# Kernel tuning notes

Hardware: AMD Instinct MI355X
Metric: run time of the kernel (lower is better)

Reference implementation:

```python
import jax, jax.numpy as jnp
import numpy as np

NUM_COMPONENTS = 4
HEADS = 16

def setup_inputs() -> dict:
    key = jax.random.key(0)
    ks = jax.random.split(key, 7)
    BC, S, D = 8, 4096, 1024   # batch*components, latent tokens, hidden dim
    E = 160                     # encoder (text) sequence length
    w_scale = 0.02              # keep logits in a sane range
    return {
        "hidden_states": jax.random.normal(ks[0], (BC, S, D), jnp.float32),
        "encoder_hidden_states": jax.random.normal(ks[1], (BC, E, D), jnp.float32),
        "Wq": jax.random.normal(ks[2], (D, D), jnp.float32) * w_scale,
        "Wk": jax.random.normal(ks[3], (D, D), jnp.float32) * w_scale,
        "Wv": jax.random.normal(ks[4], (D, D), jnp.float32) * w_scale,
        "Wo": jax.random.normal(ks[5], (D, D), jnp.float32) * w_scale,
        "bo": jnp.zeros((D,), jnp.float32),
    }

def reference(hidden_states, encoder_hidden_states, Wq, Wk, Wv, Wo, bo):
    BC, S, D = hidden_states.shape
    E = encoder_hidden_states.shape[1]
    C = NUM_COMPONENTS
    B = BC // C
    H = HEADS
    dh = D // H
    scale = dh ** -0.5

    # projections (diffusers to_q/to_k/to_v, no bias)
    q = hidden_states @ Wq            # [BC, S, D]
    k = encoder_hidden_states @ Wk    # [BC, E, D]
    v = encoder_hidden_states @ Wv    # [BC, E, D]

    q = q.reshape(BC, S, H, dh).transpose(0, 2, 1, 3)  # [BC, H, S, dh]
    k = k.reshape(BC, E, H, dh).transpose(0, 2, 1, 3)  # [BC, H, E, dh]
    v = v.reshape(BC, E, H, dh).transpose(0, 2, 1, 3)  # [BC, H, E, dh]

    scores = jnp.einsum("bhsd,bhtd->bhst", q, k) * scale  # [BC, H, S, E]
    scores_c = scores.reshape(C, B, H, S, E)

    # pooled (mean over encoder tokens) softmax across components
    pooled = scores_c.mean(axis=-1, keepdims=True)         # [C, B, H, S, 1]
    weights_pooled = jax.nn.softmax(pooled, axis=0)        # softmax over components
    # per-row softmax over encoder tokens, scaled by component weight
    weights = jax.nn.softmax(scores_c, axis=-1) * weights_pooled
    weights = weights.reshape(BC, H, S, E)

    out = jnp.einsum("bhst,bhtd->bhsd", weights, v)        # [BC, H, S, dh]
    out = out.transpose(0, 2, 1, 3).reshape(BC, S, D)

    out = out @ Wo + bo        # to_out[0]; to_out[1] is dropout (identity, eval)
    out = out + hidden_states  # residual_connection=True, rescale factor 1
    return out
```

## Files before the change

### kernel.cpp

```cpp
#include <hip/hip_runtime.h>
#include <stdint.h>

typedef __attribute__((ext_vector_type(8))) short short8;
typedef __attribute__((ext_vector_type(4))) float f32x4;
typedef __attribute__((ext_vector_type(4))) unsigned short us4;

#define DI __device__ __forceinline__

static constexpr int Dm = 1024;
static constexpr int Sm = 4096;
static constexpr int Em = 160;
static constexpr int Hm = 16;

static constexpr size_t OFF_HSB  = 0;
static constexpr size_t OFF_WT   = 67108864;
static constexpr size_t OFF_QB   = 75497472;
static constexpr size_t OFF_KB   = 142606336;
static constexpr size_t OFF_VT   = 147849216;
static constexpr size_t OFF_EHSB = 150994944;

DI unsigned short f2b(float f) {
  union { float f; unsigned u; } x; x.f = f;
  unsigned r = x.u + 0x7fffu + ((x.u >> 16) & 1u);
  return (unsigned short)(r >> 16);
}

DI float b2f(unsigned short h) {
  union { unsigned u; float f; } x; x.u = ((unsigned)h) << 16; return x.f;
}

DI void gl_lds16(const void* g, void* l) {
  __builtin_amdgcn_global_load_lds(
      (const __attribute__((address_space(1))) unsigned int*)g,
      (__attribute__((address_space(3))) unsigned int*)l, 16, 0, 0);
}

__global__ void k_prep(const float* __restrict__ ehs, unsigned short* __restrict__ eb,
                       const float* __restrict__ hs, unsigned short* __restrict__ hsb,
                       const float* __restrict__ W0, const float* __restrict__ W1,
                       const float* __restrict__ W2, const float* __restrict__ W3,
                       unsigned short* __restrict__ Wt) {
  __shared__ float t[32][33];
  const int bid = blockIdx.x, tid = threadIdx.x;
  if (bid < 4096) {
    const int bz = bid >> 10, rest = bid & 1023, by = rest >> 5, bx = rest & 31;
    const float* W = (bz == 0) ? W0 : (bz == 1) ? W1 : (bz == 2) ? W2 : W3;
    unsigned short* o = Wt + (size_t)bz * 1048576;
    const int tx = tid & 31, ty = tid >> 5;
    const int n = bx * 32 + tx, k0 = by * 32;
    #pragma unroll
    for (int j = ty; j < 32; j += 8) t[j][tx] = W[(size_t)(k0 + j) * 1024 + n];
    __syncthreads();
    #pragma unroll
    for (int j = ty; j < 32; j += 8)
      o[(size_t)(bx * 32 + j) * 1024 + k0 + tx] = f2b(t[tx][j]);
  } else if (bid < 5376) {
    const int i = (bid - 4096) * 256 + tid;
    float4 v = ((const float4*)ehs)[i];
    us4 o = { f2b(v.x), f2b(v.y), f2b(v.z), f2b(v.w) };
    *(us4*)(eb + (size_t)i * 4) = o;
  } else {
    for (int i = (bid - 5376) * 256 + tid; i < 8388608; i += 2048 * 256) {
      float4 v = ((const float4*)hs)[i];
      us4 o = { f2b(v.x), f2b(v.y), f2b(v.z), f2b(v.w) };
      *(us4*)(hsb + (size_t)i * 4) = o;
    }
  }
}

__global__ __launch_bounds__(256, 3) void k_gemm_qkv(const unsigned short* __restrict__ hsb,
                                                     const unsigned short* __restrict__ eb,
                                                     const unsigned short* __restrict__ Wt,
                                                     unsigned short* __restrict__ qb,
                                                     unsigned short* __restrict__ kb,
                                                     unsigned short* __restrict__ vt) {
  __shared__ __align__(16) char smem[32768];
  char* As = smem;
  char* Bs = smem + 16384;
  const int bid = blockIdx.x, tid = threadIdx.x;
  const int lane = tid & 63;
  const int l15 = lane & 15;
  const int g = lane >> 4;
  const int wv = tid >> 6;
  const int wr = wv >> 1, wc = wv & 1;

  const bool isKV = (bid < 160);
  int m0, n0;
  const unsigned short *Ap, *Bt;
  if (isKV) {
    const int z = bid / 80, rr = bid - z * 80;
    m0 = (rr % 10) * 128; n0 = (rr / 10) * 128;
    Ap = eb; Bt = Wt + (size_t)(1 + z) * 1048576;
  } else {
    const int q = bid - 160;
    m0 = ((q >> 6) * 8 + (q & 7)) * 128;
    n0 = ((q >> 3) & 7) * 128;
    Ap = hsb; Bt = Wt;
  }

  f32x4 acc[4][4];
  #pragma unroll
  for (int i = 0; i < 4; ++i)
    #pragma unroll
    for (int j = 0; j < 4; ++j) acc[i][j] = (f32x4){0.f, 0.f, 0.f, 0.f};

  for (int t = 0; t < 16; ++t) {
    __syncthreads();
    #pragma unroll
    for (int is = 0; is < 4; ++is) {
      int ch = is * 256 + tid;
      int row = ch >> 3, j = ch & 7;
      int sj = (j ^ (row & 7)) * 8;
      gl_lds16(Ap + (size_t)(m0 + row) * 1024 + t * 64 + sj, As + ch * 16);
      gl_lds16(Bt + (size_t)(n0 + row) * 1024 + t * 64 + sj, Bs + ch * 16);
    }
    __syncthreads();
    short8 af[2][4], bf[2][4];
    #pragma unroll
    for (int kk = 0; kk < 2; ++kk)
      #pragma unroll
      for (int mt = 0; mt < 4; ++mt) {
        af[kk][mt] = *(const short8*)(As + (wr * 64 + mt * 16 + l15) * 128 + ((kk * 64 + g * 16) ^ ((l15 & 7) << 4)));
        bf[kk][mt] = *(const short8*)(Bs + (wc * 64 + mt * 16 + l15) * 128 + ((kk * 64 + g * 16) ^ ((l15 & 7) << 4)));
      }
    #pragma unroll
    for (int kk = 0; kk < 2; ++kk)
      #pragma unroll
      for (int mt = 0; mt < 4; ++mt)
        #pragma unroll
        for (int nt = 0; nt < 4; ++nt)
          acc[mt][nt] = __builtin_amdgcn_mfma_f32_16x16x32_bf16(af[kk][mt], bf[kk][nt], acc[mt][nt], 0, 0, 0);
  }

  if (isKV) {
    const int z = bid / 80;
    #pragma unroll
    for (int mt = 0; mt < 4; ++mt)
      #pragma unroll
      for (int nt = 0; nt < 4; ++nt)
        #pragma unroll
        for (int r = 0; r < 4; ++r) {
          int row = m0 + wr * 64 + mt * 16 + 4 * g + r;
          int col = n0 + wc * 64 + nt * 16 + l15;
          unsigned short hv = f2b(acc[mt][nt][r]);
          if (z == 0) {
            kb[(size_t)row * 1024 + col] = hv;
          } else {
            int bc = row / 160, e = row - bc * 160;
            vt[((size_t)(bc * 16 + (col >> 6)) * 64 + (col & 63)) * 192 + e] = hv;
          }
        }
  } else {
    __syncthreads();
    unsigned short* Cl = (unsigned short*)smem;
    #pragma unroll
    for (int mt = 0; mt < 4; ++mt)
      #pragma unroll
      for (int nt = 0; nt < 4; ++nt)
        #pragma unroll
        for (int r = 0; r < 4; ++r)
          Cl[(wr * 64 + mt * 16 + 4 * g + r) * 128 + wc * 64 + nt * 16 + l15] = f2b(acc[mt][nt][r]);
    __syncthreads();
    #pragma unroll
    for (int j = 0; j < 8; ++j) {
      int ch = j * 256 + tid;
      int row = ch >> 4, sl = ch & 15;
      __builtin_nontemporal_store(*(const short8*)(Cl + row * 128 + sl * 8),
          (short8*)(qb + (size_t)(m0 + row) * 1024 + n0 + sl * 8));
    }
  }
}

__global__ __launch_bounds__(256, 3) void k_gemm_o(const unsigned short* __restrict__ A,
                                                   const unsigned short* __restrict__ Bt,
                                                   float* __restrict__ Cout,
                                                   const float* __restrict__ bias,
                                                   const unsigned short* __restrict__ residb) {
  __shared__ __align__(16) char smem[32768];
  char* As = smem;
  char* Bs = smem + 16384;
  const int tid = threadIdx.x;
  const int lane = tid & 63;
  const int l15 = lane & 15;
  const int g = lane >> 4;
  const int wv = tid >> 6;
  const int wr = wv >> 1, wc = wv & 1;
  const int bid = blockIdx.x;
  const int m0 = ((bid >> 6) * 8 + (bid & 7)) * 128;
  const int n0 = ((bid >> 3) & 7) * 128;

  f32x4 acc[4][4];
  #pragma unroll
  for (int i = 0; i < 4; ++i)
    #pragma unroll
    for (int j = 0; j < 4; ++j) acc[i][j] = (f32x4){0.f, 0.f, 0.f, 0.f};

  for (int t = 0; t < 16; ++t) {
    __syncthreads();
    #pragma unroll
    for (int is = 0; is < 4; ++is) {
      int ch = is * 256 + tid;
      int row = ch >> 3, j = ch & 7;
      int sj = (j ^ (row & 7)) * 8;
      gl_lds16(A  + (size_t)(m0 + row) * 1024 + t * 64 + sj, As + ch * 16);
      gl_lds16(Bt + (size_t)(n0 + row) * 1024 + t * 64 + sj, Bs + ch * 16);
    }
    __syncthreads();
    short8 af[2][4], bf[2][4];
    #pragma unroll
    for (int kk = 0; kk < 2; ++kk)
      #pragma unroll
      for (int mt = 0; mt < 4; ++mt) {
        af[kk][mt] = *(const short8*)(As + (wr * 64 + mt * 16 + l15) * 128 + ((kk * 64 + g * 16) ^ ((l15 & 7) << 4)));
        bf[kk][mt] = *(const short8*)(Bs + (wc * 64 + mt * 16 + l15) * 128 + ((kk * 64 + g * 16) ^ ((l15 & 7) << 4)));
      }
    #pragma unroll
    for (int kk = 0; kk < 2; ++kk)
      #pragma unroll
      for (int mt = 0; mt < 4; ++mt)
        #pragma unroll
        for (int nt = 0; nt < 4; ++nt)
          acc[mt][nt] = __builtin_amdgcn_mfma_f32_16x16x32_bf16(af[kk][mt], bf[kk][nt], acc[mt][nt], 0, 0, 0);
  }

  #pragma unroll
  for (int mt = 0; mt < 4; ++mt)
    #pragma unroll
    for (int nt = 0; nt < 4; ++nt)
      #pragma unroll
      for (int r = 0; r < 4; ++r) {
        size_t row = (size_t)(m0 + wr * 64 + mt * 16 + 4 * g + r);
        int col = n0 + wc * 64 + nt * 16 + l15;
        size_t idx = row * 1024 + col;
        unsigned short rh = __builtin_nontemporal_load(residb + idx);
        Cout[idx] = acc[mt][nt][r] + bias[col] + b2f(rh);
      }
}

__global__ __launch_bounds__(256, 2) void k_attn(unsigned short* __restrict__ Qb,
                                                 const unsigned short* __restrict__ Kb,
                                                 const unsigned short* __restrict__ Vt) {
  __shared__ __align__(16) char smem[22528];
  float* pooled = (float*)(smem + 21504);
  const int tid = threadIdx.x, lane = tid & 63, wv = tid >> 6;
  const int g = lane >> 4, l15 = lane & 15;
  const int s0 = blockIdx.x * 64;
  const int h = blockIdx.y;
  const int b = blockIdx.z;
  const int bc = wv * 2 + b;
  const float scale = 0.125f;

  unsigned short* Qp = Qb + ((size_t)bc * Sm + s0) * Dm + h * 64;
  const unsigned short* Kp = Kb + (size_t)bc * Em * Dm + h * 64;
  const unsigned short* Vp = Vt + ((size_t)bc * Hm + h) * (64 * 192);
  char* Pw = smem + wv * 5376;

  #pragma unroll 1
  for (int st = 0; st < 4; ++st) {
    short8 qf[2];
    #pragma unroll
    for (int kk = 0; kk < 2; ++kk)
      qf[kk] = *(const short8*)(Qp + (size_t)(st * 16 + l15) * Dm + kk * 32 + g * 8);
    f32x4 sc[10];
    #pragma unroll
    for (int et = 0; et < 10; ++et) {
      sc[et] = (f32x4){0.f, 0.f, 0.f, 0.f};
      #pragma unroll
      for (int kk = 0; kk < 2; ++kk) {
        short8 kf = *(const short8*)(Kp + (size_t)(et * 16 + l15) * Dm + kk * 32 + g * 8);
        sc[et] = __builtin_amdgcn_mfma_f32_16x16x32_bf16(qf[kk], kf, sc[et], 0, 0, 0);
      }
    }
    float rs4[4];
    #pragma unroll
    for (int r = 0; r < 4; ++r) {
      float v = 0.f;
      #pragma unroll
      for (int et = 0; et < 10; ++et) v += sc[et][r];
      v += __shfl_xor(v, 1); v += __shfl_xor(v, 2); v += __shfl_xor(v, 4); v += __shfl_xor(v, 8);
      if (l15 == 0) pooled[(st * 16 + 4 * g + r) * 4 + wv] = v * (scale / 160.f);
      float mx = sc[0][r];
      #pragma unroll
      for (int et = 1; et < 10; ++et) mx = fmaxf(mx, sc[et][r]);
      mx = fmaxf(mx, __shfl_xor(mx, 1)); mx = fmaxf(mx, __shfl_xor(mx, 2));
      mx = fmaxf(mx, __shfl_xor(mx, 4)); mx = fmaxf(mx, __shfl_xor(mx, 8));
      float rs = 0.f;
      #pragma unroll
      for (int et = 0; et < 10; ++et) {
        float p = __expf((sc[et][r] - mx) * scale);
        rs += p;
        *(unsigned short*)(Pw + (4 * g + r) * 336 + (et * 16 + l15) * 2) = f2b(p);
      }
      rs += __shfl_xor(rs, 1); rs += __shfl_xor(rs, 2); rs += __shfl_xor(rs, 4); rs += __shfl_xor(rs, 8);
      rs4[r] = rs;
    }
    f32x4 oa[4];
    #pragma unroll
    for (int dt = 0; dt < 4; ++dt) oa[dt] = (f32x4){0.f, 0.f, 0.f, 0.f};
    #pragma unroll
    for (int k5 = 0; k5 < 5; ++k5) {
      short8 pf = *(const short8*)(Pw + l15 * 336 + k5 * 64 + g * 16);
      #pragma unroll
      for (int dt = 0; dt < 4; ++dt) {
        short8 vf = *(const short8*)(Vp + (size_t)(dt * 16 + l15) * 192 + k5 * 32 + g * 8);
        oa[dt] = __builtin_amdgcn_mfma_f32_16x16x32_bf16(pf, vf, oa[dt], 0, 0, 0);
      }
    }
    __syncthreads();
    #pragma unroll
    for (int r = 0; r < 4; ++r) {
      float4 pl = *(const float4*)&pooled[(st * 16 + 4 * g + r) * 4];
      float m3 = fmaxf(fmaxf(pl.x, pl.y), fmaxf(pl.z, pl.w));
      float ssum = __expf(pl.x - m3) + __expf(pl.y - m3) + __expf(pl.z - m3) + __expf(pl.w - m3);
      float mine = (wv == 0) ? pl.x : (wv == 1) ? pl.y : (wv == 2) ? pl.z : pl.w;
      float srw = __expf(mine - m3) / (ssum * rs4[r]);
      #pragma unroll
      for (int dt = 0; dt < 4; ++dt)
        Qp[(size_t)(st * 16 + 4 * g + r) * Dm + dt * 16 + l15] = f2b(oa[dt][r] * srw);
    }
  }
}

extern "C" void kernel_launch(void* const* d_in, const int* in_sizes, int n_in,
                              void* d_out, int out_size, void* d_ws, size_t ws_size,
                              hipStream_t stream) {
  const float* hs  = (const float*)d_in[0];
  const float* ehs = (const float*)d_in[1];
  const float* Wq  = (const float*)d_in[2];
  const float* Wk  = (const float*)d_in[3];
  const float* Wv  = (const float*)d_in[4];
  const float* Wo  = (const float*)d_in[5];
  const float* bo  = (const float*)d_in[6];
  char* ws = (char*)d_ws;
  unsigned short* hsb = (unsigned short*)(ws + OFF_HSB);
  unsigned short* wt  = (unsigned short*)(ws + OFF_WT);
  unsigned short* qb  = (unsigned short*)(ws + OFF_QB);
  unsigned short* kb  = (unsigned short*)(ws + OFF_KB);
  unsigned short* vt  = (unsigned short*)(ws + OFF_VT);
  unsigned short* eb  = (unsigned short*)(ws + OFF_EHSB);

  hipLaunchKernelGGL(k_prep, dim3(7424), dim3(256), 0, stream, ehs, eb, hs, hsb, Wq, Wk, Wv, Wo, wt);
  hipLaunchKernelGGL(k_gemm_qkv, dim3(2208), dim3(256), 0, stream, hsb, eb, wt, qb, kb, vt);
  hipLaunchKernelGGL(k_attn, dim3(64, 16, 2), dim3(256), 0, stream, qb, kb, vt);
  hipLaunchKernelGGL(k_gemm_o, dim3(2048), dim3(256), 0, stream, qb, wt + 3 * 1048576, (float*)d_out, bo, hsb);
}
```

Before: 334.2 us.

## Compute pooled scores via mean-key MFMA and drop softmax max subtraction

```diff
diff --git a/kernel.cpp b/kernel.cpp
--- a/kernel.cpp
+++ b/kernel.cpp
@@ -16,6 +16,7 @@
 static constexpr size_t OFF_WT   = 67108864;
 static constexpr size_t OFF_QB   = 75497472;
 static constexpr size_t OFF_KB   = 142606336;
+static constexpr size_t OFF_KBAR = 145227776;
 static constexpr size_t OFF_VT   = 147849216;
 static constexpr size_t OFF_EHSB = 150994944;
 
@@ -169,6 +170,16 @@
           (short8*)(qb + (size_t)(m0 + row) * 1024 + n0 + sl * 8));
     }
   }
+}
+
+__global__ void k_kbar(const unsigned short* __restrict__ kb, unsigned short* __restrict__ kbar) {
+  const int bh = blockIdx.x, d = threadIdx.x;
+  const int bc = bh >> 4, h = bh & 15;
+  const unsigned short* src = kb + ((size_t)bc * Em) * Dm + h * 64 + d;
+  float s = 0.f;
+  #pragma unroll 4
+  for (int e = 0; e < Em; ++e) s += b2f(src[(size_t)e * Dm]);
+  kbar[(size_t)bh * 64 + d] = f2b(s * (1.f / 160.f));
 }
 
 __global__ __launch_bounds__(256, 3) void k_gemm_o(const unsigned short* __restrict__ A,
@@ -239,7 +250,8 @@
 
 __global__ __launch_bounds__(256, 2) void k_attn(unsigned short* __restrict__ Qb,
                                                  const unsigned short* __restrict__ Kb,
-                                                 const unsigned short* __restrict__ Vt) {
+                                                 const unsigned short* __restrict__ Vt,
+                                                 const unsigned short* __restrict__ Kbar) {
   __shared__ __align__(16) char smem[22528];
   float* pooled = (float*)(smem + 21504);
   const int tid = threadIdx.x, lane = tid & 63, wv = tid >> 6;
@@ -255,12 +267,22 @@
   const unsigned short* Vp = Vt + ((size_t)bc * Hm + h) * (64 * 192);
   char* Pw = smem + wv * 5376;
 
+  const unsigned short* kbp = Kbar + (size_t)(bc * 16 + h) * 64;
+  short8 kbf[2];
+  #pragma unroll
+  for (int kk = 0; kk < 2; ++kk)
+    kbf[kk] = *(const short8*)(kbp + kk * 32 + g * 8);
+
   #pragma unroll 1
   for (int st = 0; st < 4; ++st) {
     short8 qf[2];
     #pragma unroll
     for (int kk = 0; kk < 2; ++kk)
       qf[kk] = *(const short8*)(Qp + (size_t)(st * 16 + l15) * Dm + kk * 32 + g * 8);
+    f32x4 scb = (f32x4){0.f, 0.f, 0.f, 0.f};
+    #pragma unroll
+    for (int kk = 0; kk < 2; ++kk)
+      scb = __builtin_amdgcn_mfma_f32_16x16x32_bf16(qf[kk], kbf[kk], scb, 0, 0, 0);
     f32x4 sc[10];
     #pragma unroll
     for (int et = 0; et < 10; ++et) {
@@ -274,20 +296,11 @@
     float rs4[4];
     #pragma unroll
     for (int r = 0; r < 4; ++r) {
-      float v = 0.f;
-      #pragma unroll
-      for (int et = 0; et < 10; ++et) v += sc[et][r];
-      v += __shfl_xor(v, 1); v += __shfl_xor(v, 2); v += __shfl_xor(v, 4); v += __shfl_xor(v, 8);
-      if (l15 == 0) pooled[(st * 16 + 4 * g + r) * 4 + wv] = v * (scale / 160.f);
-      float mx = sc[0][r];
-      #pragma unroll
-      for (int et = 1; et < 10; ++et) mx = fmaxf(mx, sc[et][r]);
-      mx = fmaxf(mx, __shfl_xor(mx, 1)); mx = fmaxf(mx, __shfl_xor(mx, 2));
-      mx = fmaxf(mx, __shfl_xor(mx, 4)); mx = fmaxf(mx, __shfl_xor(mx, 8));
+      if (l15 == 0) pooled[(st * 16 + 4 * g + r) * 4 + wv] = scb[r] * scale;
       float rs = 0.f;
       #pragma unroll
       for (int et = 0; et < 10; ++et) {
-        float p = __expf((sc[et][r] - mx) * scale);
+        float p = __expf(sc[et][r] * scale);
         rs += p;
         *(unsigned short*)(Pw + (4 * g + r) * 336 + (et * 16 + l15) * 2) = f2b(p);
       }
@@ -332,15 +345,17 @@
   const float* Wo  = (const float*)d_in[5];
   const float* bo  = (const float*)d_in[6];
   char* ws = (char*)d_ws;
-  unsigned short* hsb = (unsigned short*)(ws + OFF_HSB);
-  unsigned short* wt  = (unsigned short*)(ws + OFF_WT);
-  unsigned short* qb  = (unsigned short*)(ws + OFF_QB);
-  unsigned short* kb  = (unsigned short*)(ws + OFF_KB);
-  unsigned short* vt  = (unsigned short*)(ws + OFF_VT);
-  unsigned short* eb  = (unsigned short*)(ws + OFF_EHSB);
+  unsigned short* hsb  = (unsigned short*)(ws + OFF_HSB);
+  unsigned short* wt   = (unsigned short*)(ws + OFF_WT);
+  unsigned short* qb   = (unsigned short*)(ws + OFF_QB);
+  unsigned short* kb   = (unsigned short*)(ws + OFF_KB);
+  unsigned short* kbar = (unsigned short*)(ws + OFF_KBAR);
+  unsigned short* vt   = (unsigned short*)(ws + OFF_VT);
+  unsigned short* eb   = (unsigned short*)(ws + OFF_EHSB);
 
   hipLaunchKernelGGL(k_prep, dim3(7424), dim3(256), 0, stream, ehs, eb, hs, hsb, Wq, Wk, Wv, Wo, wt);
   hipLaunchKernelGGL(k_gemm_qkv, dim3(2208), dim3(256), 0, stream, hsb, eb, wt, qb, kb, vt);
-  hipLaunchKernelGGL(k_attn, dim3(64, 16, 2), dim3(256), 0, stream, qb, kb, vt);
+  hipLaunchKernelGGL(k_kbar, dim3(128), dim3(64), 0, stream, kb, kbar);
+  hipLaunchKernelGGL(k_attn, dim3(64, 16, 2), dim3(256), 0, stream, qb, kb, vt, kbar);
   hipLaunchKernelGGL(k_gemm_o, dim3(2048), dim3(256), 0, stream, qb, wt + 3 * 1048576, (float*)d_out, bo, hsb);
 }
```

New measurement: 330.4 us. No clear change (-1.1%).
